# Performance work log

Hardware: AMD Instinct MI355X
Metric: run time of the kernel (lower is better)

## Reference

```python
import jax, jax.numpy as jnp
import numpy as np

WIN = 2  # window half-width: window = x[b, idx-2 : idx+3]

def setup_inputs() -> dict:
    key = jax.random.key(0)
    k1, k2, k3, k4 = jax.random.split(key, 4)
    B, T, C, K, H = 64, 262144, 3, 16384, 32
    x = jax.random.normal(k1, (B, T, C), dtype=jnp.float32)
    coarse_ids = jax.random.randint(k2, (B, K), 0, T, dtype=jnp.int64)
    W1 = jax.random.normal(k3, (C, H), dtype=jnp.float32) * (1.0 / np.sqrt(C))
    b1 = jnp.zeros((H,), dtype=jnp.float32)
    W2 = jax.random.normal(k4, (H, 1), dtype=jnp.float32) * (1.0 / np.sqrt(H))
    b2 = jnp.zeros((1,), dtype=jnp.float32)
    return {"x": x, "coarse_ids": coarse_ids, "W1": W1, "b1": b1, "W2": W2, "b2": b2}

def reference(x, coarse_ids, W1, b1, W2, b2):
    B, T, C = x.shape
    K = coarse_ids.shape[1]
    offsets = jnp.arange(-WIN, WIN + 1)                    # [5]
    pos = coarse_ids[:, :, None] + offsets                 # [B,K,5]
    valid = (pos >= 0) & (pos < T)                         # boundary clipping mask
    pos_c = jnp.clip(pos, 0, T - 1)
    # batched gather of 5-point windows: [B,K,5,C]
    gathered = jnp.take_along_axis(
        x, pos_c.reshape(B, K * (2 * WIN + 1), 1), axis=1
    ).reshape(B, K, 2 * WIN + 1, C)
    vf = valid.astype(x.dtype)[..., None]                  # [B,K,5,1]
    pooled = (gathered * vf).sum(axis=2) / vf.sum(axis=2)  # masked mean -> [B,K,C]
    h = jax.nn.relu(pooled @ W1 + b1)                      # [B,K,H]
    out = (h @ W2 + b2)[..., 0]                            # [B,K]
    return out
```

## Files before the change

### kernel.cpp

```cpp
#include <hip/hip_runtime.h>
#include <hip/hip_bf16.h>

#define BB 64
#define TT 262144
#define CC 3
#define KK 16384
#define HH 32
#define WIN 2

__global__ __launch_bounds__(256) void refiner_kernel(
    const float* __restrict__ x,
    const int*   __restrict__ ids,
    const float* __restrict__ W1,
    const float* __restrict__ b1,
    const float* __restrict__ W2,
    const float* __restrict__ b2,
    float*       __restrict__ out)
{
    __shared__ float sW1[CC * HH];
    __shared__ float sb1[HH];
    __shared__ float sW2[HH];
    __shared__ float sb2;

    const int t = threadIdx.x;
    if (t < CC * HH) sW1[t] = W1[t];
    if (t < HH) { sb1[t] = b1[t]; sW2[t] = W2[t]; }
    if (t == 0) sb2 = b2[0];
    __syncthreads();

    const int tid = blockIdx.x * blockDim.x + t;
    if (tid >= BB * KK) return;

    const int b   = tid >> 14;
    const int idx = ids[tid];

    const float* __restrict__ xb = x + (size_t)b * (size_t)TT * CC;

    float s0 = 0.0f, s1 = 0.0f, s2 = 0.0f, cnt = 0.0f;
#pragma unroll
    for (int o = -WIN; o <= WIN; ++o) {
        const int pos = idx + o;
        if (pos >= 0 && pos < TT) {
            const float* __restrict__ p = xb + (size_t)pos * CC;
            s0 += p[0];
            s1 += p[1];
            s2 += p[2];
            cnt += 1.0f;
        }
    }
    const float p0 = s0 / cnt;
    const float p1 = s1 / cnt;
    const float p2 = s2 / cnt;

    float acc = sb2;
#pragma unroll
    for (int j = 0; j < HH; ++j) {
        float h = fmaf(p0, sW1[j],
                  fmaf(p1, sW1[HH + j],
                  fmaf(p2, sW1[2 * HH + j], sb1[j])));
        h = h > 0.0f ? h : 0.0f;
        acc = fmaf(h, sW2[j], acc);
    }

    out[tid] = acc;
}

extern "C" void kernel_launch(void* const* d_in, const int* in_sizes, int n_in,
                              void* d_out, int out_size, void* d_ws, size_t ws_size,
                              hipStream_t stream) {
    const float* x   = (const float*)d_in[0];
    const int*   ids = (const int*)  d_in[1];
    const float* W1  = (const float*)d_in[2];
    const float* b1  = (const float*)d_in[3];
    const float* W2  = (const float*)d_in[4];
    const float* b2  = (const float*)d_in[5];
    float* out = (float*)d_out;

    const int n = BB * KK;
    const int block = 256;
    const int grid = (n + block - 1) / block;
    refiner_kernel<<<grid, block, 0, stream>>>(x, ids, W1, b1, W2, b2, out);
}
```

Measured before the change: 301.5 us.

## Vectorize interior window loads and remap blocks so each XCD owns whole batches

```diff
diff --git a/kernel.cpp b/kernel.cpp
--- a/kernel.cpp
+++ b/kernel.cpp
@@ -7,6 +7,8 @@
 #define KK 16384
 #define HH 32
 #define WIN 2
+
+typedef float f32x4 __attribute__((ext_vector_type(4), aligned(4)));
 
 __global__ __launch_bounds__(256) void refiner_kernel(
     const float* __restrict__ x,
@@ -28,29 +30,47 @@
     if (t == 0) sb2 = b2[0];
     __syncthreads();
 
-    const int tid = blockIdx.x * blockDim.x + t;
-    if (tid >= BB * KK) return;
+    const int bid   = blockIdx.x;
+    const int xcd   = bid & 7;
+    const int slot  = bid >> 3;
+    const int batch = ((slot >> 6) << 3) + xcd;
+    const int chunk = slot & 63;
+    const int tid   = batch * KK + chunk * 256 + t;
 
-    const int b   = tid >> 14;
     const int idx = ids[tid];
+    const float* __restrict__ xb = x + (size_t)batch * (size_t)TT * CC;
 
-    const float* __restrict__ xb = x + (size_t)b * (size_t)TT * CC;
-
-    float s0 = 0.0f, s1 = 0.0f, s2 = 0.0f, cnt = 0.0f;
+    float p0, p1, p2;
+    if (idx >= WIN && idx < TT - WIN) {
+        const float* base = xb + (size_t)(idx - WIN) * CC;
+        const f32x4 a = *(const f32x4*)(base);
+        const f32x4 b = *(const f32x4*)(base + 4);
+        const f32x4 c = *(const f32x4*)(base + 8);
+        const f32x4 d = *(const f32x4*)(base + 11);
+        const float s0 = a.x + a.w + b.z + c.y + d.y;
+        const float s1 = a.y + b.x + b.w + c.z + d.z;
+        const float s2 = a.z + b.y + c.x + c.w + d.w;
+        p0 = s0 * 0.2f;
+        p1 = s1 * 0.2f;
+        p2 = s2 * 0.2f;
+    } else {
+        float s0 = 0.0f, s1 = 0.0f, s2 = 0.0f, cnt = 0.0f;
 #pragma unroll
-    for (int o = -WIN; o <= WIN; ++o) {
-        const int pos = idx + o;
-        if (pos >= 0 && pos < TT) {
-            const float* __restrict__ p = xb + (size_t)pos * CC;
-            s0 += p[0];
-            s1 += p[1];
-            s2 += p[2];
-            cnt += 1.0f;
+        for (int o = -WIN; o <= WIN; ++o) {
+            const int pos = idx + o;
+            if (pos >= 0 && pos < TT) {
+                const float* p = xb + (size_t)pos * CC;
+                s0 += p[0];
+                s1 += p[1];
+                s2 += p[2];
+                cnt += 1.0f;
+            }
         }
+        const float rc = 1.0f / cnt;
+        p0 = s0 * rc;
+        p1 = s1 * rc;
+        p2 = s2 * rc;
     }
-    const float p0 = s0 / cnt;
-    const float p1 = s1 / cnt;
-    const float p2 = s2 / cnt;
 
     float acc = sb2;
 #pragma unroll
@@ -78,6 +98,6 @@
 
     const int n = BB * KK;
     const int block = 256;
-    const int grid = (n + block - 1) / block;
+    const int grid = n / block;
     refiner_kernel<<<grid, block, 0, stream>>>(x, ids, W1, b1, W2, b2, out);
 }
```

Result: faster. 268.0 us (-11.1%).

## Vectorize window loads, process two ids per thread, remap blocks to XCDs

Applied to the files above, without the earlier changes.

```diff
diff --git a/kernel.cpp b/kernel.cpp
--- a/kernel.cpp
+++ b/kernel.cpp
@@ -8,6 +8,23 @@
 #define HH 32
 #define WIN 2
 
+typedef float f32x4 __attribute__((ext_vector_type(4), aligned(4)));
+
+__device__ __forceinline__ void pool_generic(const float* __restrict__ xb, int idx,
+                                             float& p0, float& p1, float& p2) {
+    float s0 = 0.f, s1 = 0.f, s2 = 0.f, cnt = 0.f;
+#pragma unroll
+    for (int o = -WIN; o <= WIN; ++o) {
+        const int pos = idx + o;
+        if (pos >= 0 && pos < TT) {
+            const float* p = xb + (size_t)pos * CC;
+            s0 += p[0]; s1 += p[1]; s2 += p[2]; cnt += 1.f;
+        }
+    }
+    const float rc = 1.f / cnt;
+    p0 = s0 * rc; p1 = s1 * rc; p2 = s2 * rc;
+}
+
 __global__ __launch_bounds__(256) void refiner_kernel(
     const float* __restrict__ x,
     const int*   __restrict__ ids,
@@ -17,52 +34,60 @@
     const float* __restrict__ b2,
     float*       __restrict__ out)
 {
-    __shared__ float sW1[CC * HH];
-    __shared__ float sb1[HH];
-    __shared__ float sW2[HH];
-    __shared__ float sb2;
+    const int t = threadIdx.x;
 
-    const int t = threadIdx.x;
-    if (t < CC * HH) sW1[t] = W1[t];
-    if (t < HH) { sb1[t] = b1[t]; sW2[t] = W2[t]; }
-    if (t == 0) sb2 = b2[0];
-    __syncthreads();
+    const int bid   = blockIdx.x;
+    const int xcd   = bid & 7;
+    const int slot  = bid >> 3;
+    const int batch = ((slot >> 5) << 3) + xcd;
+    const int chunk = slot & 31;
+    const int pair  = batch * KK + chunk * 512 + t * 2;
 
-    const int tid = blockIdx.x * blockDim.x + t;
-    if (tid >= BB * KK) return;
+    const int2 id2 = *(const int2*)(ids + pair);
+    const float* __restrict__ xb = x + (size_t)batch * (size_t)TT * CC;
 
-    const int b   = tid >> 14;
-    const int idx = ids[tid];
+    float a0, a1, a2, c0, c1, c2;
+    const int i0 = id2.x, i1 = id2.y;
+    if (i0 >= WIN && i0 < TT - WIN && i1 >= WIN && i1 < TT - WIN) {
+        const float* ba = xb + (size_t)(i0 - WIN) * CC;
+        const float* bb = xb + (size_t)(i1 - WIN) * CC;
+        const f32x4 A0 = *(const f32x4*)(ba);
+        const f32x4 A1 = *(const f32x4*)(ba + 4);
+        const f32x4 A2 = *(const f32x4*)(ba + 8);
+        const f32x4 A3 = *(const f32x4*)(ba + 11);
+        const f32x4 B0 = *(const f32x4*)(bb);
+        const f32x4 B1 = *(const f32x4*)(bb + 4);
+        const f32x4 B2 = *(const f32x4*)(bb + 8);
+        const f32x4 B3 = *(const f32x4*)(bb + 11);
+        a0 = (A0.x + A0.w + A1.z + A2.y + A3.y) * 0.2f;
+        a1 = (A0.y + A1.x + A1.w + A2.z + A3.z) * 0.2f;
+        a2 = (A0.z + A1.y + A2.x + A2.w + A3.w) * 0.2f;
+        c0 = (B0.x + B0.w + B1.z + B2.y + B3.y) * 0.2f;
+        c1 = (B0.y + B1.x + B1.w + B2.z + B3.z) * 0.2f;
+        c2 = (B0.z + B1.y + B2.x + B2.w + B3.w) * 0.2f;
+    } else {
+        pool_generic(xb, i0, a0, a1, a2);
+        pool_generic(xb, i1, c0, c1, c2);
+    }
 
-    const float* __restrict__ xb = x + (size_t)b * (size_t)TT * CC;
-
-    float s0 = 0.0f, s1 = 0.0f, s2 = 0.0f, cnt = 0.0f;
-#pragma unroll
-    for (int o = -WIN; o <= WIN; ++o) {
-        const int pos = idx + o;
-        if (pos >= 0 && pos < TT) {
-            const float* __restrict__ p = xb + (size_t)pos * CC;
-            s0 += p[0];
-            s1 += p[1];
-            s2 += p[2];
-            cnt += 1.0f;
-        }
-    }
-    const float p0 = s0 / cnt;
-    const float p1 = s1 / cnt;
-    const float p2 = s2 / cnt;
-
-    float acc = sb2;
+    float accA = b2[0];
+    float accC = accA;
 #pragma unroll
     for (int j = 0; j < HH; ++j) {
-        float h = fmaf(p0, sW1[j],
-                  fmaf(p1, sW1[HH + j],
-                  fmaf(p2, sW1[2 * HH + j], sb1[j])));
-        h = h > 0.0f ? h : 0.0f;
-        acc = fmaf(h, sW2[j], acc);
+        const float w0 = W1[j];
+        const float w1 = W1[HH + j];
+        const float w2 = W1[2 * HH + j];
+        const float bj = b1[j];
+        const float vj = W2[j];
+        float hA = fmaf(a0, w0, fmaf(a1, w1, fmaf(a2, w2, bj)));
+        float hC = fmaf(c0, w0, fmaf(c1, w1, fmaf(c2, w2, bj)));
+        hA = fmaxf(hA, 0.f);
+        hC = fmaxf(hC, 0.f);
+        accA = fmaf(hA, vj, accA);
+        accC = fmaf(hC, vj, accC);
     }
 
-    out[tid] = acc;
+    *(float2*)(out + pair) = make_float2(accA, accC);
 }
 
 extern "C" void kernel_launch(void* const* d_in, const int* in_sizes, int n_in,
@@ -78,6 +103,6 @@
 
     const int n = BB * KK;
     const int block = 256;
-    const int grid = (n + block - 1) / block;
+    const int grid = n / (block * 2);
     refiner_kernel<<<grid, block, 0, stream>>>(x, ids, W1, b1, W2, b2, out);
 }
```

Result: faster. 267.4 us (-11.3%).
